# Optimization experiments

Measured on AMD Instinct MI355X. Metric: run time of the kernel, lower is better.

## Reference

```python
import jax, jax.numpy as jnp
import numpy as np

B, NT, D, V = 16, 4096, 512, 2545  # batch, text len, text_dim, text_num_embeds


def setup_inputs() -> dict:
    key = jax.random.key(0)
    k_txt, k_len, k_emb = jax.random.split(key, 3)
    text = jax.random.randint(k_txt, (B, NT), 0, V, dtype=jnp.int64)
    # ragged valid lengths; pad tail with -1 (-> token 0 after +1 shift)
    lengths = jax.random.randint(k_len, (B,), 1, NT + 1, dtype=jnp.int64)
    pos = jnp.arange(NT, dtype=jnp.int64)
    text = jnp.where(pos[None, :] < lengths[:, None], text, -1)
    emb = jax.random.normal(k_emb, (V + 1, D), dtype=jnp.float32) * 0.02
    return {"text": text, "seq_len": 4096, "emb": emb}


def _forward(emb, text, seq_len):
    t = text + 1
    t = t[:, :seq_len]
    t = jnp.pad(t, ((0, 0), (0, seq_len - t.shape[1])))  # pad with 0
    pad_mask = t == 0                      # [b, s] True at padding
    x = emb[t]                             # [b, s, d] embedding lookup
    # --- average upsample by valid mask (vectorized replacement of the
    #     per-batch Python loop in average_upsample_text_by_mask) ---
    valid = ~pad_mask
    L = valid.sum(axis=1)                  # [b] valid token counts
    # stable argsort of ~valid puts valid positions first, in order
    order = jnp.argsort(~valid, axis=1, stable=True)        # [b, s]
    gathered = jnp.take_along_axis(x, order[:, :, None], axis=1)  # [b, s, d]
    Ls = jnp.maximum(L, 1)
    base = seq_len // Ls                   # [b]
    rem = seq_len % Ls                     # [b]
    # token j repeats base times for j < L-rem, base+1 times for j >= L-rem
    pos = jnp.arange(seq_len, dtype=L.dtype)                # [s]
    boundary = (Ls - rem) * base           # [b] first output pos of the +1 block
    j_lo = pos[None, :] // base[:, None]
    j_hi = (Ls - rem)[:, None] + (pos[None, :] - boundary[:, None]) // (base + 1)[:, None]
    j = jnp.where(pos[None, :] < boundary[:, None], j_lo, j_hi)  # [b, s]
    out = jnp.take_along_axis(gathered, j[:, :, None], axis=1)   # [b, s, d]
    out = jnp.where((L == 0)[:, None, None], jnp.zeros((), out.dtype), out)
    return out


def reference(text, seq_len, emb):
    return _forward(emb, text, seq_len)
```

## Files before the change

### kernel.cpp

```cpp
#include <hip/hip_runtime.h>
#include <hip/hip_bf16.h>

#define B_   16
#define NT_  4096
#define D_   512

typedef float f4 __attribute__((ext_vector_type(4)));

__global__ __launch_bounds__(256) void expand_fused(const int* __restrict__ text,
                                                    const f4* __restrict__ emb,
                                                    f4* __restrict__ out) {
    const int gpos = blockIdx.x * 4;
    const int b    = gpos >> 12;
    const int wid  = threadIdx.x >> 6;
    const int lane = threadIdx.x & 63;
    const int p    = (gpos & (NT_ - 1)) + wid;

    const int* __restrict__ row = text + b * NT_;

    int lo = 0, hi = NT_;
    while (lo < hi) {
        const int mid = (lo + hi) >> 1;
        if (row[mid] >= 0) lo = mid + 1; else hi = mid;
    }
    const int L = lo;

    const int Ls       = (L > 0) ? L : 1;
    const int base     = NT_ / Ls;
    const int rem      = NT_ - base * Ls;
    const int boundary = (Ls - rem) * base;
    const int j = (p < boundary) ? (p / base)
                                 : ((Ls - rem) + (p - boundary) / (base + 1));

    f4 v0, v1;
    if (L == 0) {
        v0 = (f4)0.f;
        v1 = (f4)0.f;
    } else {
        const int tkn = row[j] + 1;
        const f4* __restrict__ erow = emb + (size_t)tkn * (D_ / 4);
        v0 = erow[lane * 2];
        v1 = erow[lane * 2 + 1];
    }
    f4* orow = out + (size_t)(gpos + wid) * (D_ / 4);
    __builtin_nontemporal_store(v0, &orow[lane * 2]);
    __builtin_nontemporal_store(v1, &orow[lane * 2 + 1]);
}

extern "C" void kernel_launch(void* const* d_in, const int* in_sizes, int n_in,
                              void* d_out, int out_size, void* d_ws, size_t ws_size,
                              hipStream_t stream) {
    const int*   text = (const int*)d_in[0];
    const float* emb  = (const float*)d_in[2];
    float*       out  = (float*)d_out;

    expand_fused<<<(B_ * NT_) / 4, 256, 0, stream>>>(
        text, (const f4*)emb, (f4*)out);
}
```

Baseline: 172.7 us.

## Split into token-map precompute kernel and flat embedding expand kernel

Splits the fused kernel in two. The first kernel runs once per batch row: it does the binary search for the valid length a single time and writes the source token for every output position into workspace. The second kernel is a flat gather in which each thread copies one f4 of an embedding row, using regular stores instead of nontemporal ones. This removes the redundant per-wave binary search and index math, but adds a second launch, a workspace round-trip and smaller per-thread work.

```diff
diff --git a/kernel.cpp b/kernel.cpp
--- a/kernel.cpp
+++ b/kernel.cpp
@@ -7,44 +7,62 @@
 
 typedef float f4 __attribute__((ext_vector_type(4)));
 
-__global__ __launch_bounds__(256) void expand_fused(const int* __restrict__ text,
-                                                    const f4* __restrict__ emb,
-                                                    f4* __restrict__ out) {
-    const int gpos = blockIdx.x * 4;
-    const int b    = gpos >> 12;
-    const int wid  = threadIdx.x >> 6;
-    const int lane = threadIdx.x & 63;
-    const int p    = (gpos & (NT_ - 1)) + wid;
-
+__global__ __launch_bounds__(256) void map_kernel(const int* __restrict__ text,
+                                                  int* __restrict__ exp_tok) {
+    const int b = blockIdx.x;
+    const int t = threadIdx.x;
     const int* __restrict__ row = text + b * NT_;
 
-    int lo = 0, hi = NT_;
-    while (lo < hi) {
-        const int mid = (lo + hi) >> 1;
-        if (row[mid] >= 0) lo = mid + 1; else hi = mid;
+    __shared__ int s_meta[4];
+    if (t == 0) {
+        int lo = 0, hi = NT_;
+        while (lo < hi) {
+            const int mid = (lo + hi) >> 1;
+            if (row[mid] >= 0) lo = mid + 1; else hi = mid;
+        }
+        const int L  = lo;
+        const int Ls = (L > 0) ? L : 1;
+        const int base = NT_ / Ls;
+        const int rem  = NT_ - base * Ls;
+        s_meta[0] = L;
+        s_meta[1] = base;
+        s_meta[2] = rem;
+        s_meta[3] = (Ls - rem) * base;
     }
-    const int L = lo;
+    __syncthreads();
+    const int L        = s_meta[0];
+    const int base     = s_meta[1];
+    const int rem      = s_meta[2];
+    const int boundary = s_meta[3];
+    const int Ls       = (L > 0) ? L : 1;
 
-    const int Ls       = (L > 0) ? L : 1;
-    const int base     = NT_ / Ls;
-    const int rem      = NT_ - base * Ls;
-    const int boundary = (Ls - rem) * base;
-    const int j = (p < boundary) ? (p / base)
-                                 : ((Ls - rem) + (p - boundary) / (base + 1));
+    #pragma unroll
+    for (int k = 0; k < NT_ / 256; ++k) {
+        const int p = t + k * 256;
+        int token = -1;
+        if (L > 0) {
+            const int j = (p < boundary) ? (p / base)
+                                         : ((Ls - rem) + (p - boundary) / (base + 1));
+            token = row[j] + 1;
+        }
+        exp_tok[b * NT_ + p] = token;
+    }
+}
 
-    f4 v0, v1;
-    if (L == 0) {
-        v0 = (f4)0.f;
-        v1 = (f4)0.f;
+__global__ __launch_bounds__(256) void expand_kernel(const f4* __restrict__ emb,
+                                                     const int* __restrict__ exp_tok,
+                                                     f4* __restrict__ out) {
+    const int tid  = blockIdx.x * 256 + threadIdx.x;
+    const int pidx = tid >> 7;
+    const int d4   = tid & 127;
+    const int tkn  = exp_tok[pidx];
+    f4 v;
+    if (tkn < 0) {
+        v = (f4)0.f;
     } else {
-        const int tkn = row[j] + 1;
-        const f4* __restrict__ erow = emb + (size_t)tkn * (D_ / 4);
-        v0 = erow[lane * 2];
-        v1 = erow[lane * 2 + 1];
+        v = emb[(size_t)tkn * (D_ / 4) + d4];
     }
-    f4* orow = out + (size_t)(gpos + wid) * (D_ / 4);
-    __builtin_nontemporal_store(v0, &orow[lane * 2]);
-    __builtin_nontemporal_store(v1, &orow[lane * 2 + 1]);
+    out[tid] = v;
 }
 
 extern "C" void kernel_launch(void* const* d_in, const int* in_sizes, int n_in,
@@ -54,6 +72,9 @@
     const float* emb  = (const float*)d_in[2];
     float*       out  = (float*)d_out;
 
-    expand_fused<<<(B_ * NT_) / 4, 256, 0, stream>>>(
-        text, (const f4*)emb, (f4*)out);
+    int* exp_tok = (int*)d_ws;
+
+    map_kernel<<<B_, 256, 0, stream>>>(text, exp_tok);
+    expand_kernel<<<(B_ * NT_ * (D_ / 4)) / 256, 256, 0, stream>>>(
+        (const f4*)emb, exp_tok, (f4*)out);
 }
```

After: 160.9 us. 6.8% less time.
